# Kernel optimization log

Measured on AMD Instinct MI355X. Metric: run time of the kernel, lower is better.

## Reference

```python
import jax, jax.numpy as jnp
import numpy as np

NUM_HEADS = 8
DIM_HEAD_QK = 32
DIM_HEAD_V = 32
BLOCK = 8
HALO = 3
WIN = BLOCK + 2 * HALO  # 14
SCALE = DIM_HEAD_QK ** -0.5


def rel_logits_1d(q, rel_k, permute_mask):
    N, H, W, d = q.shape
    rel_size = rel_k.shape[0]
    win = (rel_size + 1) // 2
    x = jnp.einsum('nhwd,rd->nhwr', q, rel_k)
    x = x.reshape(N * H, W, rel_size)
    x = jnp.pad(x, ((0, 0), (0, 0), (0, 1))).reshape(N * H, -1)
    x = jnp.pad(x, ((0, 0), (0, rel_size - W)))
    x = x.reshape(N * H, W + 1, rel_size)[:, :W, win - 1:]
    x = jnp.broadcast_to(x.reshape(N, H, 1, W, win), (N, H, win, W, win))
    return jnp.transpose(x, permute_mask)


def pos_embed_rel(q, height_rel, width_rel):
    BH, NB, HW, d = q.shape
    qb = q.reshape(-1, BLOCK, BLOCK, d)
    rel_w = rel_logits_1d(qb, width_rel, (0, 1, 3, 2, 4))
    rel_h = rel_logits_1d(jnp.swapaxes(qb, 1, 2), height_rel, (0, 3, 1, 4, 2))
    return (rel_h + rel_w).reshape(BH, NB, HW, WIN * WIN)


def reference(x, q_weight, kv_weight, height_rel, width_rel):
    B, C, H, W = x.shape
    nhb, nwb = H // BLOCK, W // BLOCK
    nb = nhb * nwb
    # 1x1 conv projections
    q = jnp.einsum('bchw,oc->bohw', x, q_weight)
    q = q.reshape(B * NUM_HEADS, DIM_HEAD_QK, nhb, BLOCK, nwb, BLOCK)
    q = jnp.transpose(q, (0, 1, 3, 5, 2, 4)).reshape(B * NUM_HEADS, DIM_HEAD_QK, BLOCK * BLOCK, nb)
    q = jnp.swapaxes(q, 1, 3)  # (BH, nb, BLOCK*BLOCK, dhq)
    kv = jnp.einsum('bchw,oc->bohw', x, kv_weight)
    kv = jnp.pad(kv, ((0, 0), (0, 0), (HALO, HALO), (HALO, HALO)))
    # halo windows: overlapping WINxWIN patches strided by BLOCK
    h_idx = jnp.arange(nhb)[:, None] * BLOCK + jnp.arange(WIN)[None, :]
    w_idx = jnp.arange(nwb)[:, None] * BLOCK + jnp.arange(WIN)[None, :]
    kv = kv[:, :, h_idx, :][:, :, :, :, w_idx]
    kv = jnp.transpose(kv, (0, 1, 2, 4, 3, 5)).reshape(
        B * NUM_HEADS, DIM_HEAD_QK + DIM_HEAD_V, nb, WIN * WIN)
    kv = jnp.transpose(kv, (0, 2, 3, 1))
    k, v = kv[..., :DIM_HEAD_QK], kv[..., DIM_HEAD_QK:]
    attn = jnp.einsum('bnqd,bnkd->bnqk', q, k) * SCALE
    attn = attn + pos_embed_rel(q, height_rel, width_rel)
    attn = jax.nn.softmax(attn, axis=-1)
    out = jnp.einsum('bnqk,bnkd->bnqd', attn, v)
    out = jnp.swapaxes(out, 1, 3)  # (BH, dhv, BLOCK*BLOCK, nb)
    out = out.reshape(-1, BLOCK, BLOCK, nhb, nwb)
    out = jnp.transpose(out, (0, 3, 1, 4, 2)).reshape(B, NUM_HEADS * DIM_HEAD_V, H, W)
    return out


def setup_inputs() -> dict:
    key = jax.random.key(0)
    k1, k2, k3, k4, k5 = jax.random.split(key, 5)
    dim = 256
    std = dim ** -0.5
    x = jax.random.normal(k1, (8, 256, 96, 96), dtype=jnp.float32)
    q_weight = jax.random.normal(k2, (256, 256), dtype=jnp.float32) * std
    kv_weight = jax.random.normal(k3, (512, 256), dtype=jnp.float32) * std
    height_rel = jax.random.normal(k4, (2 * WIN - 1, DIM_HEAD_QK), dtype=jnp.float32) * SCALE
    width_rel = jax.random.normal(k5, (2 * WIN - 1, DIM_HEAD_QK), dtype=jnp.float32) * SCALE
    return {'x': x, 'q_weight': q_weight, 'kv_weight': kv_weight,
            'height_rel': height_rel, 'width_rel': width_rel}
```

## Files before the change

### kernel.cpp

```cpp
#include <hip/hip_runtime.h>
#include <math.h>

#define NPIX 9216
#define SCALE 0.17677669529663687f
#define LOG2E 1.4426950408889634f

typedef __attribute__((ext_vector_type(8))) short bh8;
typedef __attribute__((ext_vector_type(4))) float f4;

__device__ __forceinline__ unsigned short f2bf(float f) {
    unsigned u = __float_as_uint(f);
    u += 0x7fff + ((u >> 16) & 1);
    return (unsigned short)(u >> 16);
}
__device__ __forceinline__ void gload_lds16(const void* g, void* l) {
    __builtin_amdgcn_global_load_lds(
        (const __attribute__((address_space(1))) unsigned int*)g,
        (__attribute__((address_space(3))) unsigned int*)l, 16, 0, 0);
}

__global__ void wconv_kernel(const float* __restrict__ qw, const float* __restrict__ kvw,
                             const float* __restrict__ hrel, const float* __restrict__ wrel,
                             unsigned short* __restrict__ Wb,
                             unsigned short* __restrict__ relb) {
    int bid = blockIdx.x, tid = threadIdx.x;
    if (bid < 768) {
        float v = (bid < 256) ? qw[bid * 256 + tid] : kvw[(bid - 256) * 256 + tid];
        Wb[bid * 256 + tid] = f2bf(v);
    } else {
        int e = (bid - 768) * 256 + tid;
        int half = e >> 10, r = (e >> 5) & 31, d = e & 31;
        float v = 0.0f;
        if (r < 27) v = (half ? wrel : hrel)[r * 32 + d] * LOG2E;
        relb[half * 1024 + r * 32 + d] = f2bf(v);
    }
}

__global__ __launch_bounds__(256) void xtrans_kernel(const float* __restrict__ x,
                                                     unsigned short* __restrict__ xt) {
    int b = blockIdx.z;
    int p0 = blockIdx.x * 128, c0 = blockIdx.y * 128;
    int tid = threadIdx.x;
    __shared__ __align__(16) unsigned short ts[128 * 136];
    const float* xb = x + (size_t)b * 256 * NPIX;
    #pragma unroll
    for (int it = 0; it < 16; ++it) {
        int e = it * 256 + tid;
        int ch = e >> 5, p4 = (e & 31) * 4;
        float4 v = *(const float4*)(xb + (size_t)(c0 + ch) * NPIX + p0 + p4);
        ts[(p4 + 0) * 136 + ch] = f2bf(v.x);
        ts[(p4 + 1) * 136 + ch] = f2bf(v.y);
        ts[(p4 + 2) * 136 + ch] = f2bf(v.z);
        ts[(p4 + 3) * 136 + ch] = f2bf(v.w);
    }
    __syncthreads();
    unsigned short* xtb = xt + (size_t)b * NPIX * 256;
    #pragma unroll
    for (int it = 0; it < 8; ++it) {
        int e = it * 256 + tid;
        int p = e >> 4, ck = (e & 15) * 8;
        *(int4*)(xtb + (size_t)(p0 + p) * 256 + c0 + ck) = *(const int4*)&ts[p * 136 + ck];
    }
}

__global__ __launch_bounds__(256) void proj_kernel(const unsigned short* __restrict__ xt,
                                                   const unsigned short* __restrict__ Wb,
                                                   unsigned short* __restrict__ qb,
                                                   unsigned short* __restrict__ kvb) {
    int b = blockIdx.z;
    int m0 = blockIdx.x * 128;
    int n0 = blockIdx.y * 128;
    int tid = threadIdx.x, lane = tid & 63, wave = tid >> 6;
    __shared__ __align__(16) char smem[32768];
    char* As = smem;
    char* Bs = smem + 16384;
    const unsigned short* xtb = xt + (size_t)b * NPIX * 256;

    f4 acc[4][4] = {};
    int wm = (wave & 1) * 64, wn = (wave >> 1) * 64;

    for (int k0 = 0; k0 < 256; k0 += 64) {
        __syncthreads();
        #pragma unroll
        for (int i = 0; i < 4; ++i) {
            int c = wave * 4 + i;
            gload_lds16(xtb + (size_t)(m0 + c * 8 + (lane >> 3)) * 256 + k0 + (lane & 7) * 8,
                        As + c * 1024);
            gload_lds16(Wb + (size_t)(n0 + c * 8 + (lane >> 3)) * 256 + k0 + (lane & 7) * 8,
                        Bs + c * 1024);
        }
        __syncthreads();
        #pragma unroll
        for (int ks = 0; ks < 2; ++ks) {
            bh8 af[4], bf[4];
            #pragma unroll
            for (int i = 0; i < 4; ++i)
                af[i] = *(const bh8*)(As + (wm + i * 16 + (lane & 15)) * 128 + ks * 64 + (lane >> 4) * 16);
            #pragma unroll
            for (int j = 0; j < 4; ++j)
                bf[j] = *(const bh8*)(Bs + (wn + j * 16 + (lane & 15)) * 128 + ks * 64 + (lane >> 4) * 16);
            #pragma unroll
            for (int i = 0; i < 4; ++i)
                #pragma unroll
                for (int j = 0; j < 4; ++j)
                    acc[i][j] = __builtin_amdgcn_mfma_f32_16x16x32_bf16(af[i], bf[j], acc[i][j], 0, 0, 0);
        }
    }

    bool isQ = (n0 < 256);
    int q4 = (lane >> 4) * 4;
    #pragma unroll
    for (int i = 0; i < 4; ++i) {
        #pragma unroll
        for (int j = 0; j < 4; ++j) {
            int ch = n0 + wn + j * 16 + (lane & 15);
            #pragma unroll
            for (int r = 0; r < 4; ++r) {
                int pix = m0 + wm + i * 16 + q4 + r;
                unsigned short v = f2bf(acc[i][j][r]);
                if (isQ) {
                    int head = ch >> 5, d = ch & 31;
                    qb[((size_t)(b * 8 + head) * NPIX + pix) * 32 + d] = v;
                } else {
                    int c = ch - 256, head = c >> 6, dv = c & 63;
                    kvb[((size_t)(b * 8 + head) * NPIX + pix) * 64 + dv] = v;
                }
            }
        }
    }
}

__global__ __launch_bounds__(256) void attn_kernel(const unsigned short* __restrict__ qbuf,
                                                   const unsigned short* __restrict__ kvbuf,
                                                   const unsigned short* __restrict__ relb,
                                                   float* __restrict__ out) {
    int nbid = blockIdx.x, bh = blockIdx.y;
    int b = bh >> 3, head = bh & 7;
    int hb = nbid / 12, wblk = nbid % 12;
    int r0 = hb * 8, c0 = wblk * 8;
    int tid = threadIdx.x, lane = tid & 63, wave = tid >> 6;
    int ll = lane & 15, lq = lane >> 4;
    int m0 = wave * 16;

    __shared__ __align__(16) char smem[50368];
    unsigned short* Vt = (unsigned short*)smem;
    unsigned short* Ks = (unsigned short*)(smem + 15360);
    float*          RhT = (float*)(smem + 33280);
    float*          Rw  = (float*)(smem + 40896);
    unsigned short* Ps  = (unsigned short*)(smem + 15360 + wave * 7424);
    float*          smR = (float*)(smem + 50112);

    const unsigned short* qb  = qbuf  + (size_t)bh * NPIX * 32;
    const unsigned short* kvb = kvbuf + (size_t)bh * NPIX * 64;

    int qp0 = m0 + ll;
    int pixq = (r0 + (qp0 >> 3)) * 96 + c0 + (qp0 & 7);
    bh8 aq = *(const bh8*)&qb[(size_t)pixq * 32 + lq * 8];

    for (int e = tid; e < 896; e += 256) {
        int kp = e >> 2, part = e & 3;
        int a = kp >> 4, b2 = kp & 15;
        int gr = r0 + a - 3, gc = c0 + b2 - 3;
        int4 v = {0, 0, 0, 0};
        if (b2 < 14 && (unsigned)gr < 96u && (unsigned)gc < 96u)
            v = *(const int4*)&kvb[(size_t)(gr * 96 + gc) * 64 + part * 8];
        *(int4*)&Ks[kp * 40 + part * 8] = v;
    }

    #pragma unroll
    for (int it = 0; it < 2; ++it) {
        int e = it * 256 + tid;
        int part = e >> 7, kp2 = e & 127;
        if (kp2 < 112) {
            int a = kp2 >> 3, b2 = (kp2 & 7) * 2;
            int gr = r0 + a - 3, gc = c0 + b2 - 3;
            int4 lo = {0, 0, 0, 0}, hi = {0, 0, 0, 0};
            bool rok = ((kp2 & 7) < 7) && ((unsigned)gr < 96u);
            if (rok && (unsigned)gc < 96u)
                lo = *(const int4*)&kvb[(size_t)(gr * 96 + gc) * 64 + 32 + part * 8];
            if (rok && (unsigned)(gc + 1) < 96u)
                hi = *(const int4*)&kvb[(size_t)(gr * 96 + gc + 1) * 64 + 32 + part * 8];
            int g = kp2 >> 2, kb = b2 & 7;
            const unsigned* lw = (const unsigned*)&lo;
            const unsigned* hw = (const unsigned*)&hi;
            #pragma unroll
            for (int jw = 0; jw < 4; ++jw) {
                unsigned l2 = lw[jw], h2 = hw[jw];
                unsigned v0 = (l2 & 0xffffu) | (h2 << 16);
                unsigned v1 = (l2 >> 16) | (h2 & 0xffff0000u);
                int d0 = part * 8 + jw * 2;
                int s0 = (((jw * 2) & 3) + part) & 3;
                int s1 = (((jw * 2 + 1) & 3) + part) & 3;
                *(unsigned*)&Vt[d0 * 240 + ((g ^ s0) * 8) + kb] = v0;
                *(unsigned*)&Vt[(d0 + 1) * 240 + ((g ^ s1) * 8) + kb] = v1;
            }
        }
    }

    f4 zero4 = {0.f, 0.f, 0.f, 0.f};
    #pragma unroll
    for (int t = 0; t < 2; ++t) {
        int r = t * 16 + ll;
        bh8 hbv = *(const bh8*)&relb[(size_t)r * 32 + lq * 8];
        bh8 wbv = *(const bh8*)&relb[1024 + (size_t)r * 32 + lq * 8];
        f4 ch = __builtin_amdgcn_mfma_f32_16x16x32_bf16(aq, hbv, zero4, 0, 0, 0);
        f4 cw = __builtin_amdgcn_mfma_f32_16x16x32_bf16(aq, wbv, zero4, 0, 0, 0);
        if (r < 28) *(f4*)&RhT[r * 68 + m0 + lq * 4] = ch;
        #pragma unroll
        for (int rr = 0; rr < 4; ++rr)
            Rw[(m0 + lq * 4 + rr) * 36 + r] = cw[rr];
    }

    __syncthreads();

    f4 S[14];
    #pragma unroll
    for (int t = 0; t < 14; ++t) {
        bh8 bk = *(const bh8*)&Ks[(t * 16 + ll) * 40 + lq * 8];
        S[t] = __builtin_amdgcn_mfma_f32_16x16x32_bf16(aq, bk, zero4, 0, 0, 0);
    }

    int row0 = m0 + lq * 4;
    int h = row0 >> 3;
    float rw4[4];
    #pragma unroll
    for (int rr = 0; rr < 4; ++rr) {
        int row = row0 + rr;
        rw4[rr] = Rw[row * 36 + 13 + ll - (row & 7)];
    }
    const float SL = SCALE * LOG2E;
    bool valid = ll < 14;
    float sm4[4] = {0.f, 0.f, 0.f, 0.f};
    #pragma unroll
    for (int t = 0; t < 14; ++t) {
        f4 rh = *(const f4*)&RhT[(13 + t - h) * 68 + row0];
        #pragma unroll
        for (int rr = 0; rr < 4; ++rr) {
            float lg = S[t][rr] * SL + rh[rr] + rw4[rr];
            float p = valid ? __builtin_amdgcn_exp2f(lg) : 0.0f;
            S[t][rr] = p;
            sm4[rr] += p;
        }
    }
    #pragma unroll
    for (int rr = 0; rr < 4; ++rr) {
        sm4[rr] += __shfl_xor(sm4[rr], 1);
        sm4[rr] += __shfl_xor(sm4[rr], 2);
        sm4[rr] += __shfl_xor(sm4[rr], 4);
        sm4[rr] += __shfl_xor(sm4[rr], 8);
    }
    if (ll == 0) {
        #pragma unroll
        for (int rr = 0; rr < 4; ++rr) smR[row0 + rr] = sm4[rr];
    }

    __syncthreads();

    #pragma unroll
    for (int t = 0; t < 14; ++t) {
        int col = t * 16 + ll;
        #pragma unroll
        for (int rr = 0; rr < 4; ++rr)
            Ps[(lq * 4 + rr) * 232 + col] = f2bf(S[t][rr]);
    }

    f4 O[2] = {zero4, zero4};
    #pragma unroll
    for (int kt = 0; kt < 7; ++kt) {
        bh8 bp = *(const bh8*)&Ps[ll * 232 + kt * 32 + lq * 8];
        #pragma unroll
        for (int mt = 0; mt < 2; ++mt) {
            int d = mt * 16 + ll;
            int s = ((d & 3) + ((d >> 3) & 3)) & 3;
            bh8 av = *(const bh8*)&Vt[d * 240 + (((kt * 4 + lq) ^ s) * 8)];
            O[mt] = __builtin_amdgcn_mfma_f32_16x16x32_bf16(av, bp, O[mt], 0, 0, 0);
        }
    }

    int qp = m0 + ll;
    float rs = 1.0f / smR[qp];
    int pix = (r0 + (qp >> 3)) * 96 + c0 + (qp & 7);
    float* ob = out + (size_t)(b * 256 + head * 32) * NPIX;
    #pragma unroll
    for (int mt = 0; mt < 2; ++mt) {
        #pragma unroll
        for (int rr = 0; rr < 4; ++rr) {
            int d = mt * 16 + lq * 4 + rr;
            ob[(size_t)d * NPIX + pix] = O[mt][rr] * rs;
        }
    }
}

extern "C" void kernel_launch(void* const* d_in, const int* in_sizes, int n_in,
                              void* d_out, int out_size, void* d_ws, size_t ws_size,
                              hipStream_t stream) {
    const float* x    = (const float*)d_in[0];
    const float* qw   = (const float*)d_in[1];
    const float* kvw  = (const float*)d_in[2];
    const float* hrel = (const float*)d_in[3];
    const float* wrel = (const float*)d_in[4];
    float* out = (float*)d_out;

    char* ws = (char*)d_ws;
    unsigned short* xt    = (unsigned short*)ws;
    unsigned short* Wb    = (unsigned short*)(ws + 37748736);
    unsigned short* relb  = (unsigned short*)(ws + 38141952);
    unsigned short* qbuf  = (unsigned short*)(ws + 38146048);
    unsigned short* kvbuf = (unsigned short*)(ws + 75894784);

    wconv_kernel<<<dim3(776), 256, 0, stream>>>(qw, kvw, hrel, wrel, Wb, relb);
    xtrans_kernel<<<dim3(72, 2, 8), 256, 0, stream>>>(x, xt);
    proj_kernel<<<dim3(72, 6, 8), 256, 0, stream>>>(xt, Wb, qbuf, kvbuf);
    attn_kernel<<<dim3(144, 64), 256, 0, stream>>>(qbuf, kvbuf, relb, out);
}
```

Before: 279.5 us.

## Stage projection output through LDS for vector stores and swizzle block order

The projection epilogue now writes bf16 results into a padded LDS tile and then emits 16-byte vector stores to the q/kv buffers, replacing scattered 2-byte global writes. Both the projection and attention kernels remap the flat block index so that consecutive blocks are interleaved across eight groups, changing which blocks run concurrently, likely to spread work across XCDs or improve cache locality. The attention softmax folds the invalid-column mask into the rel-width bias as -inf, removing a per-element select. The price is an extra LDS round trip and barrier in the projection kernel, plus slightly more shared memory.

```diff
diff --git a/kernel.cpp b/kernel.cpp
--- a/kernel.cpp
+++ b/kernel.cpp
@@ -67,11 +67,14 @@
                                                    const unsigned short* __restrict__ Wb,
                                                    unsigned short* __restrict__ qb,
                                                    unsigned short* __restrict__ kvb) {
-    int b = blockIdx.z;
-    int m0 = blockIdx.x * 128;
-    int n0 = blockIdx.y * 128;
+    int flat = blockIdx.x + 72 * (blockIdx.y + 6 * blockIdx.z);
+    int w = (flat & 7) * 432 + (flat >> 3);
+    int n0 = (w % 6) * 128;
+    int m0 = ((w / 6) % 72) * 128;
+    int b  = w / 432;
     int tid = threadIdx.x, lane = tid & 63, wave = tid >> 6;
-    __shared__ __align__(16) char smem[32768];
+    int ll = lane & 15;
+    __shared__ __align__(16) char smem[34816];
     char* As = smem;
     char* Bs = smem + 16384;
     const unsigned short* xtb = xt + (size_t)b * NPIX * 256;
@@ -95,10 +98,10 @@
             bh8 af[4], bf[4];
             #pragma unroll
             for (int i = 0; i < 4; ++i)
-                af[i] = *(const bh8*)(As + (wm + i * 16 + (lane & 15)) * 128 + ks * 64 + (lane >> 4) * 16);
+                af[i] = *(const bh8*)(As + (wm + i * 16 + ll) * 128 + ks * 64 + (lane >> 4) * 16);
             #pragma unroll
             for (int j = 0; j < 4; ++j)
-                bf[j] = *(const bh8*)(Bs + (wn + j * 16 + (lane & 15)) * 128 + ks * 64 + (lane >> 4) * 16);
+                bf[j] = *(const bh8*)(Bs + (wn + j * 16 + ll) * 128 + ks * 64 + (lane >> 4) * 16);
             #pragma unroll
             for (int i = 0; i < 4; ++i)
                 #pragma unroll
@@ -107,25 +110,33 @@
         }
     }
 
+    __syncthreads();
+    unsigned short* ts = (unsigned short*)smem;
+    int q4 = (lane >> 4) * 4;
+    #pragma unroll
+    for (int i = 0; i < 4; ++i) {
+        #pragma unroll
+        for (int j = 0; j < 4; ++j) {
+            int ch = wn + j * 16 + ll;
+            #pragma unroll
+            for (int r = 0; r < 4; ++r)
+                ts[(wm + i * 16 + q4 + r) * 136 + ch] = f2bf(acc[i][j][r]);
+        }
+    }
+    __syncthreads();
     bool isQ = (n0 < 256);
-    int q4 = (lane >> 4) * 4;
-    #pragma unroll
-    for (int i = 0; i < 4; ++i) {
-        #pragma unroll
-        for (int j = 0; j < 4; ++j) {
-            int ch = n0 + wn + j * 16 + (lane & 15);
-            #pragma unroll
-            for (int r = 0; r < 4; ++r) {
-                int pix = m0 + wm + i * 16 + q4 + r;
-                unsigned short v = f2bf(acc[i][j][r]);
-                if (isQ) {
-                    int head = ch >> 5, d = ch & 31;
-                    qb[((size_t)(b * 8 + head) * NPIX + pix) * 32 + d] = v;
-                } else {
-                    int c = ch - 256, head = c >> 6, dv = c & 63;
-                    kvb[((size_t)(b * 8 + head) * NPIX + pix) * 64 + dv] = v;
-                }
-            }
+    #pragma unroll
+    for (int it = 0; it < 8; ++it) {
+        int e = it * 256 + tid;
+        int pixl = e >> 4, ck = (e & 15) * 8;
+        int4 v = *(const int4*)&ts[pixl * 136 + ck];
+        int pix = m0 + pixl, ch = n0 + ck;
+        if (isQ) {
+            int head = ch >> 5, d = ch & 31;
+            *(int4*)&qb[((size_t)(b * 8 + head) * NPIX + pix) * 32 + d] = v;
+        } else {
+            int c = ch - 256, head = c >> 6, dv = c & 63;
+            *(int4*)&kvb[((size_t)(b * 8 + head) * NPIX + pix) * 64 + dv] = v;
         }
     }
 }
@@ -134,7 +145,9 @@
                                                    const unsigned short* __restrict__ kvbuf,
                                                    const unsigned short* __restrict__ relb,
                                                    float* __restrict__ out) {
-    int nbid = blockIdx.x, bh = blockIdx.y;
+    int flat = blockIdx.x + 144 * blockIdx.y;
+    int w = (flat & 7) * 1152 + (flat >> 3);
+    int nbid = w % 144, bh = w / 144;
     int b = bh >> 3, head = bh & 7;
     int hb = nbid / 12, wblk = nbid % 12;
     int r0 = hb * 8, c0 = wblk * 8;
@@ -222,14 +235,14 @@
 
     int row0 = m0 + lq * 4;
     int h = row0 >> 3;
+    float nv = (ll < 14) ? 0.0f : -INFINITY;
     float rw4[4];
     #pragma unroll
     for (int rr = 0; rr < 4; ++rr) {
         int row = row0 + rr;
-        rw4[rr] = Rw[row * 36 + 13 + ll - (row & 7)];
+        rw4[rr] = Rw[row * 36 + 13 + ll - (row & 7)] + nv;
     }
     const float SL = SCALE * LOG2E;
-    bool valid = ll < 14;
     float sm4[4] = {0.f, 0.f, 0.f, 0.f};
     #pragma unroll
     for (int t = 0; t < 14; ++t) {
@@ -237,7 +250,7 @@
         #pragma unroll
         for (int rr = 0; rr < 4; ++rr) {
             float lg = S[t][rr] * SL + rh[rr] + rw4[rr];
-            float p = valid ? __builtin_amdgcn_exp2f(lg) : 0.0f;
+            float p = __builtin_amdgcn_exp2f(lg);
             S[t][rr] = p;
             sm4[rr] += p;
         }
```

Result: faster. 273.2 us (-2.2%).
